# Kernel optimization log

Measured on AMD Instinct MI355X. Metric: run time of the kernel, lower is better.

The kernel has to match this reference:

```python
import jax, jax.numpy as jnp
import numpy as np

N = 100000      # number of entities
E = 400000      # number of edges (before self-loops)
D = 200         # feature_dim
D0 = 100        # init_fea_dim
NREL = 475      # 2*num_rels + 1 (self-loop relation = NREL-1)
NBR = 100       # num_base_r
B = 1024        # query batch
L = 2           # number of cells / layers
EPS = 1e-5


def _bn(x, g, b):
    # BatchNorm1d, training-mode batch statistics (biased var), per-feature affine
    m = jnp.mean(x, axis=0)
    v = jnp.var(x, axis=0)
    return (x - m) * jax.lax.rsqrt(v + EPS) * g + b


def setup_inputs() -> dict:
    key = jax.random.key(0)
    ks = jax.random.split(key, 12)
    return {
        # graph (edge list form of the DGL graph g)
        "src_id": jax.random.randint(ks[0], (E,), 0, N),
        "dst_id": jax.random.randint(ks[1], (E,), 0, N),
        "e_type": jax.random.randint(ks[2], (E,), 0, NREL - 1),  # NREL-1 reserved for self-loop
        # link-prediction queries
        "subj": jax.random.randint(ks[3], (B,), 0, N),
        "rel": jax.random.randint(ks[4], (B,), 0, NREL),
        # learned parameters
        "emb_h": jax.random.normal(ks[5], (N, D0), dtype=jnp.float32) * 0.02,
        "emb_e": jax.random.normal(ks[6], (NBR, D), dtype=jnp.float32) * 0.1,
        "lin_w": jax.random.normal(ks[7], (D0, D), dtype=jnp.float32) * (1.0 / np.sqrt(D0)),
        "lin_b": jnp.zeros((D,), dtype=jnp.float32),
        "rel_wt": jax.random.normal(ks[8], (NREL, NBR), dtype=jnp.float32) * 0.1,
        "w_rel": jax.random.normal(ks[9], (D, D), dtype=jnp.float32) * (1.0 / np.sqrt(D)),
        # per-cell params, stacked over L layers
        "agg_bn_g": jnp.ones((L, D), dtype=jnp.float32),
        "agg_bn_b": jnp.zeros((L, D), dtype=jnp.float32),
        "cell_bn_g": jnp.ones((L, D), dtype=jnp.float32),
        "cell_bn_b": jnp.zeros((L, D), dtype=jnp.float32),
        "concat_w": jax.random.normal(ks[10], (L, D, D), dtype=jnp.float32) * (1.0 / np.sqrt(D)),
        "concat_b": jnp.zeros((L, D), dtype=jnp.float32),
    }


def reference(src_id, dst_id, e_type, subj, rel,
              emb_h, emb_e, lin_w, lin_b, rel_wt, w_rel,
              agg_bn_g, agg_bn_b, cell_bn_g, cell_bn_b, concat_w, concat_b):
    nodes = jnp.arange(N, dtype=src_id.dtype)
    # append self-loops for every node, with the dedicated self-loop relation id
    src_f = jnp.concatenate([src_id, nodes])                      # [E+N]
    dst_f = jnp.concatenate([dst_id, nodes])                      # [E+N]
    et_f = jnp.concatenate([e_type, jnp.full((N,), NREL - 1, dtype=e_type.dtype)])

    all_ent = emb_h @ lin_w + lin_b                               # [N, D]
    rel_embed = rel_wt @ emb_e                                    # [NREL, D]

    for i in range(L):
        src_emb = all_ent[src_f]                                  # [E+N, D] per-edge gather
        hr = rel_embed[et_f]                                      # [E+N, D] per-edge gather
        zero_out = src_emb * hr                                   # pre_mult op (no BN/ReLU)
        agg = jax.ops.segment_sum(zero_out, dst_f, num_segments=N)  # edge -> node aggregation
        agg = jax.nn.relu(_bn(agg, agg_bn_g[i], agg_bn_b[i]))     # OpModule BN + ReLU
        h = agg @ concat_w[i] + concat_b[i]                       # Cell concat Linear (1 concat node)
        all_ent = jax.nn.relu(_bn(h, cell_bn_g[i], cell_bn_b[i]))  # Cell BN + ReLU
        rel_embed = rel_embed @ w_rel                             # per-layer relation transform

    # DistMult score function: [B, N]
    score = (all_ent[subj] * rel_embed[rel]) @ all_ent.T
    return score
```

## Files before the change

kernel.cpp:

```cpp
#include <hip/hip_runtime.h>


#define N_ENT  100000
#define N_EDGE 400000
#define D_     200
#define D0_    100
#define NREL_  475
#define B_     1024
#define GSTAT2 2048
#define KP_D   224
#define KP_D0  128

typedef unsigned short ushort_t;
typedef __attribute__((ext_vector_type(8))) short bf16x8;
typedef __attribute__((ext_vector_type(4))) float f32x4;

__device__ __forceinline__ ushort_t f2bf(float x) {
  unsigned u = __float_as_uint(x);
  return (ushort_t)((u + 0x7FFFu + ((u >> 16) & 1u)) >> 16);
}
__device__ __forceinline__ float bf2f(ushort_t h) {
  return __uint_as_float(((unsigned)h) << 16);
}

__device__ __forceinline__ void gld16(const void* g, void* l) {
  __builtin_amdgcn_global_load_lds(
      (const __attribute__((address_space(1))) unsigned*)g,
      (__attribute__((address_space(3))) unsigned*)l, 16, 0, 0);
}


__global__ void k_hist(const int* __restrict__ dst_id, int* __restrict__ cnt) {
  int e = blockIdx.x * 256 + threadIdx.x;
  if (e < N_EDGE) atomicAdd(&cnt[dst_id[e]], 1);
}

__global__ __launch_bounds__(256) void k_scan_block(const int* __restrict__ cnt,
                                                    int* __restrict__ rp,
                                                    int* __restrict__ bsum) {
  __shared__ int sm[256];
  int tid = threadIdx.x;
  int base = blockIdx.x * 1024 + tid * 4;
  int v0 = (base + 0 < N_ENT) ? cnt[base + 0] : 0;
  int v1 = (base + 1 < N_ENT) ? cnt[base + 1] : 0;
  int v2 = (base + 2 < N_ENT) ? cnt[base + 2] : 0;
  int v3 = (base + 3 < N_ENT) ? cnt[base + 3] : 0;
  int tsum = v0 + v1 + v2 + v3;
  sm[tid] = tsum;
  __syncthreads();
  for (int off = 1; off < 256; off <<= 1) {
    int t = (tid >= off) ? sm[tid - off] : 0;
    __syncthreads();
    sm[tid] += t;
    __syncthreads();
  }
  int run = sm[tid] - tsum;
  if (base + 0 < N_ENT) { rp[base + 0] = run; } run += v0;
  if (base + 1 < N_ENT) { rp[base + 1] = run; } run += v1;
  if (base + 2 < N_ENT) { rp[base + 2] = run; } run += v2;
  if (base + 3 < N_ENT) { rp[base + 3] = run; }
  if (tid == 255) bsum[blockIdx.x] = sm[255];
}

__global__ void k_scan_tops(int* __restrict__ bsum, int nb) {
  __shared__ int sm[256];
  int tid = threadIdx.x;
  int v = (tid < nb) ? bsum[tid] : 0;
  sm[tid] = v;
  __syncthreads();
  for (int off = 1; off < 256; off <<= 1) {
    int t = (tid >= off) ? sm[tid - off] : 0;
    __syncthreads();
    sm[tid] += t;
    __syncthreads();
  }
  if (tid < nb) bsum[tid] = sm[tid] - v;
}

__global__ void k_scan_add(int* __restrict__ rp, const int* __restrict__ bsum,
                           int* __restrict__ cursor) {
  int i = blockIdx.x * 256 + threadIdx.x;
  if (i < N_ENT) {
    int r = rp[i] + bsum[i >> 10];
    rp[i] = r;
    cursor[i] = r;
  }
}

__global__ void k_fill(const int* __restrict__ src_id, const int* __restrict__ dst_id,
                       const int* __restrict__ e_type, int* __restrict__ cursor,
                       int* __restrict__ cs, int* __restrict__ ct) {
  int e = blockIdx.x * 256 + threadIdx.x;
  if (e < N_EDGE) {
    int pos = atomicAdd(&cursor[dst_id[e]], 1);
    cs[pos] = src_id[e];
    ct[pos] = e_type[e];
  }
}


template <bool BN>
__global__ __launch_bounds__(256) void k_aggregate(const float* __restrict__ ent,
                                                   const float* __restrict__ relE,
                                                   const int* __restrict__ rp,
                                                   const int* __restrict__ cnt,
                                                   const int* __restrict__ cs,
                                                   const int* __restrict__ ct,
                                                   float* __restrict__ out,
                                                   const float* __restrict__ scale,
                                                   const float* __restrict__ shift) {
  const int wv = threadIdx.x >> 6;
  const int lane = threadIdx.x & 63;
  const int n = blockIdx.x * 4 + wv;
  if (n >= N_ENT || lane >= 50) return;
  const int f4 = lane * 4;

  float sc[4] = {0, 0, 0, 0}, sh[4] = {0, 0, 0, 0};
  if (BN) {
    float4 s4 = *(const float4*)(scale + f4);
    float4 h4 = *(const float4*)(shift + f4);
    sc[0] = s4.x; sc[1] = s4.y; sc[2] = s4.z; sc[3] = s4.w;
    sh[0] = h4.x; sh[1] = h4.y; sh[2] = h4.z; sh[3] = h4.w;
  }

  float ax[4], ay[4] = {0, 0, 0, 0};
  {
    float4 e = *(const float4*)(ent + (long)n * D_ + f4);
    float4 r = *(const float4*)(relE + (long)(NREL_ - 1) * D_ + f4);
    float ee[4] = {e.x, e.y, e.z, e.w};
    float rr[4] = {r.x, r.y, r.z, r.w};
#pragma unroll
    for (int u = 0; u < 4; ++u) {
      if (BN) ee[u] = fmaxf(fmaf(ee[u], sc[u], sh[u]), 0.f);
      ax[u] = ee[u] * rr[u];
    }
  }

  int s0 = rp[n], e0 = s0 + cnt[n];
  int idx = s0;
  for (; idx + 2 <= e0; idx += 2) {
    int sA = cs[idx], tA = ct[idx];
    int sB = cs[idx + 1], tB = ct[idx + 1];
    float4 eA = *(const float4*)(ent + (long)sA * D_ + f4);
    float4 rA = *(const float4*)(relE + (long)tA * D_ + f4);
    float4 eB = *(const float4*)(ent + (long)sB * D_ + f4);
    float4 rB = *(const float4*)(relE + (long)tB * D_ + f4);
    float ea[4] = {eA.x, eA.y, eA.z, eA.w}, ra[4] = {rA.x, rA.y, rA.z, rA.w};
    float eb[4] = {eB.x, eB.y, eB.z, eB.w}, rb[4] = {rB.x, rB.y, rB.z, rB.w};
#pragma unroll
    for (int u = 0; u < 4; ++u) {
      if (BN) {
        ea[u] = fmaxf(fmaf(ea[u], sc[u], sh[u]), 0.f);
        eb[u] = fmaxf(fmaf(eb[u], sc[u], sh[u]), 0.f);
      }
      ax[u] = fmaf(ea[u], ra[u], ax[u]);
      ay[u] = fmaf(eb[u], rb[u], ay[u]);
    }
  }
  if (idx < e0) {
    int sA = cs[idx], tA = ct[idx];
    float4 eA = *(const float4*)(ent + (long)sA * D_ + f4);
    float4 rA = *(const float4*)(relE + (long)tA * D_ + f4);
    float ea[4] = {eA.x, eA.y, eA.z, eA.w}, ra[4] = {rA.x, rA.y, rA.z, rA.w};
#pragma unroll
    for (int u = 0; u < 4; ++u) {
      if (BN) ea[u] = fmaxf(fmaf(ea[u], sc[u], sh[u]), 0.f);
      ax[u] = fmaf(ea[u], ra[u], ax[u]);
    }
  }
  float4 o = make_float4(ax[0] + ay[0], ax[1] + ay[1], ax[2] + ay[2], ax[3] + ay[3]);
  *(float4*)(out + (long)n * D_ + f4) = o;
}

__global__ __launch_bounds__(64) void k_colstats(const float* __restrict__ X,
                                                 double* __restrict__ part) {
  int t = threadIdx.x;
  if (t >= 50) return;
  double s0 = 0, s1 = 0, s2 = 0, s3 = 0, q0 = 0, q1 = 0, q2 = 0, q3 = 0;
  for (int r = blockIdx.x; r < N_ENT; r += GSTAT2) {
    float4 v = *(const float4*)(X + (long)r * D_ + t * 4);
    s0 += v.x; q0 += (double)v.x * v.x;
    s1 += v.y; q1 += (double)v.y * v.y;
    s2 += v.z; q2 += (double)v.z * v.z;
    s3 += v.w; q3 += (double)v.w * v.w;
  }
  long o = (long)blockIdx.x * 400 + t * 4;
  part[o + 0] = s0; part[o + 1] = s1; part[o + 2] = s2; part[o + 3] = s3;
  part[o + 200] = q0; part[o + 201] = q1; part[o + 202] = q2; part[o + 203] = q3;
}

__global__ __launch_bounds__(256) void k_bn_fin(const double* __restrict__ part,
                                                const float* __restrict__ g,
                                                const float* __restrict__ b,
                                                float* __restrict__ scale,
                                                float* __restrict__ shift) {
  int f = blockIdx.x;
  int tid = threadIdx.x;
  double S = 0.0, S2 = 0.0;
  for (int i = tid; i < GSTAT2; i += 256) {
    S += part[(long)i * 400 + f];
    S2 += part[(long)i * 400 + 200 + f];
  }
  __shared__ double smS[256], smS2[256];
  smS[tid] = S; smS2[tid] = S2;
  __syncthreads();
  for (int off = 128; off > 0; off >>= 1) {
    if (tid < off) { smS[tid] += smS[tid + off]; smS2[tid] += smS2[tid + off]; }
    __syncthreads();
  }
  if (tid == 0) {
    double mean = smS[0] / N_ENT;
    double var = smS2[0] / N_ENT - mean * mean;
    double inv = 1.0 / sqrt(var + 1e-5);
    float sc = g[f] * (float)inv;
    scale[f] = sc;
    shift[f] = b[f] - (float)mean * sc;
  }
}

__global__ void k_norm_split(float* __restrict__ X, const float* __restrict__ scale,
                             const float* __restrict__ shift,
                             ushort_t* __restrict__ H, ushort_t* __restrict__ L) {
  const long total = (long)N_ENT * (KP_D / 4);
  for (long i4 = (long)blockIdx.x * 256 + threadIdx.x; i4 < total;
       i4 += (long)gridDim.x * 256) {
    int r = (int)(i4 / (KP_D / 4));
    int c4 = (int)(i4 % (KP_D / 4)) * 4;
    float vv[4] = {0.f, 0.f, 0.f, 0.f};
    if (c4 < D_) {
      float4 v = *(float4*)(X + (long)r * D_ + c4);
      vv[0] = fmaxf(fmaf(v.x, scale[c4 + 0], shift[c4 + 0]), 0.f);
      vv[1] = fmaxf(fmaf(v.y, scale[c4 + 1], shift[c4 + 1]), 0.f);
      vv[2] = fmaxf(fmaf(v.z, scale[c4 + 2], shift[c4 + 2]), 0.f);
      vv[3] = fmaxf(fmaf(v.w, scale[c4 + 3], shift[c4 + 3]), 0.f);
      *(float4*)(X + (long)r * D_ + c4) = make_float4(vv[0], vv[1], vv[2], vv[3]);
    }
    ushort_t h[4], l[4];
#pragma unroll
    for (int t = 0; t < 4; t++) {
      h[t] = f2bf(vv[t]);
      l[t] = f2bf(vv[t] - bf2f(h[t]));
    }
    long o = (long)r * KP_D + c4;
    *(uint2*)(H + o) = make_uint2((unsigned)h[0] | ((unsigned)h[1] << 16),
                                  (unsigned)h[2] | ((unsigned)h[3] << 16));
    *(uint2*)(L + o) = make_uint2((unsigned)l[0] | ((unsigned)l[1] << 16),
                                  (unsigned)l[2] | ((unsigned)l[3] << 16));
  }
}

__global__ void k_tsplit(const float* __restrict__ W, int K, int Nc, int Kp,
                         ushort_t* __restrict__ H, ushort_t* __restrict__ L) {
  int i = blockIdx.x * 256 + threadIdx.x;
  if (i >= Nc * Kp) return;
  int n = i / Kp, kp = i - n * Kp;
  float v = (kp < K) ? W[(long)kp * Nc + n] : 0.f;
  ushort_t h = f2bf(v);
  H[i] = h;
  L[i] = f2bf(v - bf2f(h));
}

__global__ void k_qsplit(const float* __restrict__ ent, const float* __restrict__ relE,
                         const int* __restrict__ subj, const int* __restrict__ rel,
                         ushort_t* __restrict__ H, ushort_t* __restrict__ L) {
  int i = blockIdx.x * 256 + threadIdx.x;
  if (i >= B_ * KP_D) return;
  int b = i / KP_D, kp = i - b * KP_D;
  float v = 0.f;
  if (kp < D_)
    v = ent[(long)subj[b] * D_ + kp] * relE[(long)rel[b] * D_ + kp];
  ushort_t h = f2bf(v);
  H[i] = h;
  L[i] = f2bf(v - bf2f(h));
}

__global__ __launch_bounds__(256, 2) void k_score4(
    const ushort_t* __restrict__ Ah, const ushort_t* __restrict__ Al,
    const ushort_t* __restrict__ Bh, const ushort_t* __restrict__ Bl,
    float* __restrict__ C) {
  constexpr int KP = KP_D;
  __shared__ __align__(16) ushort_t lds[2 * 14336];
  const int tid = threadIdx.x;
  const int wave = tid >> 6, lane = tid & 63;
  const int l15 = lane & 15, l4 = lane >> 4;

  int g = (blockIdx.x & 7) * 1563 + (blockIdx.x >> 3);
  const int bm = (g & 7) * 128;
  const int bn = (g >> 3) * 64;

  bf16x8 qh[2][7], ql[2][7];
#pragma unroll
  for (int i = 0; i < 2; ++i) {
    long rowa = (long)(bm + wave * 32 + i * 16 + l15) * KP + l4 * 8;
#pragma unroll
    for (int k = 0; k < 7; ++k) {
      qh[i][k] = *(const bf16x8*)(Ah + rowa + k * 32);
      ql[i][k] = *(const bf16x8*)(Al + rowa + k * 32);
    }
  }

#pragma unroll
  for (int jj = 0; jj < 14; ++jj) {
    int c = wave * 14 + jj;
    int u = c * 64 + lane;
    int isl = (u >= 1792) ? 1 : 0;
    int u2 = u - isl * 1792;
    int kst = u2 >> 8;
    int rem = u2 & 255;
    int r = rem >> 2;
    int slot = rem & 3;
    int srcslot = slot ^ ((r >> 1) & 3);
    int rowg = bn + r; if (rowg > N_ENT - 1) rowg = N_ENT - 1;
    const ushort_t* src = (isl ? Bl : Bh) + (long)rowg * KP + kst * 32 + srcslot * 8;
    gld16(src, lds + c * 512);
  }
  __syncthreads();

  f32x4 acc[2][4] = {};
#pragma unroll
  for (int k = 0; k < 7; ++k) {
    bf16x8 eh[4], el[4];
#pragma unroll
    for (int j = 0; j < 4; ++j) {
      int rB = j * 16 + l15;
      int slot = l4 ^ ((rB >> 1) & 3);
      int ad = k * 2048 + rB * 32 + slot * 8;
      eh[j] = *(const bf16x8*)(lds + ad);
      el[j] = *(const bf16x8*)(lds + 14336 + ad);
    }
#pragma unroll
    for (int i = 0; i < 2; ++i)
#pragma unroll
      for (int j = 0; j < 4; ++j) {
        acc[i][j] = __builtin_amdgcn_mfma_f32_16x16x32_bf16(eh[j], qh[i][k], acc[i][j], 0, 0, 0);
        acc[i][j] = __builtin_amdgcn_mfma_f32_16x16x32_bf16(eh[j], ql[i][k], acc[i][j], 0, 0, 0);
        acc[i][j] = __builtin_amdgcn_mfma_f32_16x16x32_bf16(el[j], qh[i][k], acc[i][j], 0, 0, 0);
      }
  }

#pragma unroll
  for (int i = 0; i < 2; ++i) {
    int m = bm + wave * 32 + i * 16 + l15;
#pragma unroll
    for (int j = 0; j < 4; ++j) {
      int nb = bn + j * 16 + l4 * 4;
      if (nb < N_ENT) {
        float4 o = make_float4(acc[i][j][0], acc[i][j][1], acc[i][j][2], acc[i][j][3]);
        *(float4*)(C + (long)m * N_ENT + nb) = o;
      }
    }
  }
}

template <bool BN_A, bool HAS_BIAS>
__global__ __launch_bounds__(256, 2) void k_mfma_af32(
    const float* __restrict__ A, int lda, int K,
    const ushort_t* __restrict__ Bh, const ushort_t* __restrict__ Bl,
    float* __restrict__ C, int M, int Nc, int Kp, long ldc,
    const float* __restrict__ scale, const float* __restrict__ shift,
    const float* __restrict__ bias) {
  __shared__ __align__(16) ushort_t lds[2 * 16384];
  __shared__ float sc_lds[KP_D], sh_lds[KP_D];
  const int tid = threadIdx.x;
  const int wave = tid >> 6, lane = tid & 63;
  const int bm = blockIdx.x * 128, bn = blockIdx.y * 128;
  const int wr = (wave >> 1) * 64, wc = (wave & 1) * 64;
  const int l15 = lane & 15, l4 = lane >> 4;
  const int NT = Kp >> 5;

  if (BN_A) {
    for (int i = tid; i < Kp; i += 256) {
      sc_lds[i] = (i < K) ? scale[i] : 0.f;
      sh_lds[i] = (i < K) ? shift[i] : 0.f;
    }
    __syncthreads();
  }

  const int ar = tid >> 1;
  const int acb = (tid & 1) * 16;
  int arow = bm + ar; if (arow > M - 1) arow = M - 1;
  const int aswz = (ar >> 1) & 3;
  const int s0 = (((acb >> 3) + 0) ^ aswz) * 8;
  const int s1 = (((acb >> 3) + 1) ^ aswz) * 8;

  auto loadA = [&](int kt, float4* va) {
    int kc = kt * 32 + acb;
    const float* ap = A + (long)arow * lda + kc;
    if (kc + 16 <= K) {
#pragma unroll
      for (int q = 0; q < 4; q++) va[q] = *(const float4*)(ap + q * 4);
    } else {
#pragma unroll
      for (int q = 0; q < 4; q++) {
        float t0 = (kc + q * 4 + 0 < K) ? ap[q * 4 + 0] : 0.f;
        float t1 = (kc + q * 4 + 1 < K) ? ap[q * 4 + 1] : 0.f;
        float t2 = (kc + q * 4 + 2 < K) ? ap[q * 4 + 2] : 0.f;
        float t3 = (kc + q * 4 + 3 < K) ? ap[q * 4 + 3] : 0.f;
        va[q] = make_float4(t0, t1, t2, t3);
      }
    }
  };

  auto writeA = [&](int kt, int ph, float4* va) {
    float v[16];
#pragma unroll
    for (int q = 0; q < 4; q++) {
      v[q * 4 + 0] = va[q].x; v[q * 4 + 1] = va[q].y;
      v[q * 4 + 2] = va[q].z; v[q * 4 + 3] = va[q].w;
    }
    if (BN_A) {
      int kc = kt * 32 + acb;
#pragma unroll
      for (int e = 0; e < 16; e++) {
        int col = kc + e;
        if (col < K) v[e] = fmaxf(fmaf(v[e], sc_lds[col], sh_lds[col]), 0.f);
      }
    }
    unsigned hh[8], ll[8];
#pragma unroll
    for (int e = 0; e < 8; e++) {
      ushort_t h0 = f2bf(v[2 * e]), h1 = f2bf(v[2 * e + 1]);
      ushort_t l0 = f2bf(v[2 * e] - bf2f(h0)), l1 = f2bf(v[2 * e + 1] - bf2f(h1));
      hh[e] = (unsigned)h0 | ((unsigned)h1 << 16);
      ll[e] = (unsigned)l0 | ((unsigned)l1 << 16);
    }
    ushort_t* baseA = lds + ph * 16384 + ar * 32;
    *(uint4*)(baseA + s0) = make_uint4(hh[0], hh[1], hh[2], hh[3]);
    *(uint4*)(baseA + s1) = make_uint4(hh[4], hh[5], hh[6], hh[7]);
    ushort_t* baseL = baseA + 4096;
    *(uint4*)(baseL + s0) = make_uint4(ll[0], ll[1], ll[2], ll[3]);
    *(uint4*)(baseL + s1) = make_uint4(ll[4], ll[5], ll[6], ll[7]);
  };

  auto stageB = [&](int kt, int ph) {
#pragma unroll
    for (int j = 0; j < 4; ++j) {
      int c = 16 + wave * 4 + j;
      int buf = c >> 3;
      int r = (c & 7) * 16 + (lane >> 2);
      int sg = (lane & 3) ^ ((r >> 1) & 3);
      const ushort_t* bp = (buf == 2) ? Bh : Bl;
      int rowg = bn + r; if (rowg > Nc - 1) rowg = Nc - 1;
      gld16(bp + (long)rowg * Kp + kt * 32 + sg * 8, lds + ph * 16384 + c * 512);
    }
  };

  f32x4 acc[4][4] = {};
  {
    float4 va[4];
    loadA(0, va);
    writeA(0, 0, va);
    stageB(0, 0);
  }
  __syncthreads();
  int p = 0;
  for (int t = 0; t < NT; ++t) {
    float4 va[4];
    const bool pre = (t + 1 < NT);
    if (pre) {
      loadA(t + 1, va);
      stageB(t + 1, p ^ 1);
    }
    const ushort_t* base = lds + p * 16384;
    bf16x8 a_h[4], a_l[4], b_h[4], b_l[4];
#pragma unroll
    for (int i = 0; i < 4; i++) {
      int rA = wr + i * 16 + l15;
      int sA = (l4 ^ ((rA >> 1) & 3)) * 8;
      a_h[i] = *(const bf16x8*)(base + rA * 32 + sA);
      a_l[i] = *(const bf16x8*)(base + 4096 + rA * 32 + sA);
      int rB = wc + i * 16 + l15;
      int sB = (l4 ^ ((rB >> 1) & 3)) * 8;
      b_h[i] = *(const bf16x8*)(base + 8192 + rB * 32 + sB);
      b_l[i] = *(const bf16x8*)(base + 12288 + rB * 32 + sB);
    }
#pragma unroll
    for (int i = 0; i < 4; i++)
#pragma unroll
      for (int j = 0; j < 4; j++) {
        acc[i][j] = __builtin_amdgcn_mfma_f32_16x16x32_bf16(a_h[i], b_h[j], acc[i][j], 0, 0, 0);
        acc[i][j] = __builtin_amdgcn_mfma_f32_16x16x32_bf16(a_l[i], b_h[j], acc[i][j], 0, 0, 0);
        acc[i][j] = __builtin_amdgcn_mfma_f32_16x16x32_bf16(a_h[i], b_l[j], acc[i][j], 0, 0, 0);
      }
    if (pre) writeA(t + 1, p ^ 1, va);
    __syncthreads();
    p ^= 1;
  }

#pragma unroll
  for (int i = 0; i < 4; i++) {
    int mrow = bm + wr + i * 16 + l4 * 4;
#pragma unroll
    for (int j = 0; j < 4; j++) {
      int n = bn + wc + j * 16 + l15;
      if (n >= Nc) continue;
      float bb = HAS_BIAS ? bias[n] : 0.f;
#pragma unroll
      for (int v = 0; v < 4; v++) {
        int m = mrow + v;
        if (m < M) C[(long)m * ldc + n] = acc[i][j][v] + bb;
      }
    }
  }
}

template <int TM, int TN>
__global__ __launch_bounds__(256) void k_gemm_abt(
    const float* __restrict__ A, const float* __restrict__ Bm, float* __restrict__ C,
    int M, int Nc, int K, long ldc) {
  constexpr int BM = TM * 16, BN = TN * 16, KC = 20;
  __shared__ float As[BM * KC];
  __shared__ float Bs[BN * KC];
  const int tid = threadIdx.x;
  const int tx = tid & 15, ty = tid >> 4;
  const int bm = blockIdx.x * BM, bn = blockIdx.y * BN;
  float acc[TM][TN];
#pragma unroll
  for (int i = 0; i < TM; i++)
#pragma unroll
    for (int j = 0; j < TN; j++) acc[i][j] = 0.f;
  for (int kc = 0; kc < K; kc += KC) {
    for (int i4 = tid; i4 < BM * 5; i4 += 256) {
      int r = i4 / 5, kq = (i4 - r * 5) * 4;
      int row = bm + r; if (row > M - 1) row = M - 1;
      *(float4*)(As + r * KC + kq) = *(const float4*)(A + (long)row * K + kc + kq);
    }
    for (int i4 = tid; i4 < BN * 5; i4 += 256) {
      int r = i4 / 5, kq = (i4 - r * 5) * 4;
      int row = bn + r; if (row > Nc - 1) row = Nc - 1;
      *(float4*)(Bs + r * KC + kq) = *(const float4*)(Bm + (long)row * K + kc + kq);
    }
    __syncthreads();
#pragma unroll
    for (int k4 = 0; k4 < KC; k4 += 4) {
      float4 af[TM], bf[TN];
#pragma unroll
      for (int i = 0; i < TM; i++) af[i] = *(const float4*)(As + (i * 16 + ty) * KC + k4);
#pragma unroll
      for (int j = 0; j < TN; j++) bf[j] = *(const float4*)(Bs + (j * 16 + tx) * KC + k4);
#pragma unroll
      for (int i = 0; i < TM; i++)
#pragma unroll
        for (int j = 0; j < TN; j++) {
          acc[i][j] = fmaf(af[i].x, bf[j].x, acc[i][j]);
          acc[i][j] = fmaf(af[i].y, bf[j].y, acc[i][j]);
          acc[i][j] = fmaf(af[i].z, bf[j].z, acc[i][j]);
          acc[i][j] = fmaf(af[i].w, bf[j].w, acc[i][j]);
        }
    }
    __syncthreads();
  }
#pragma unroll
  for (int i = 0; i < TM; i++) {
    int m = bm + i * 16 + ty;
    if (m >= M) continue;
#pragma unroll
    for (int j = 0; j < TN; j++) {
      int n = bn + j * 16 + tx;
      if (n < Nc) C[(long)m * ldc + n] = acc[i][j];
    }
  }
}

__global__ void k_transpose(const float* __restrict__ s, float* __restrict__ d, int R, int C) {
  int i = blockIdx.x * 256 + threadIdx.x;
  if (i < R * C) { int r = i / C, c = i - r * C; d[c * R + r] = s[i]; }
}


extern "C" void kernel_launch(void* const* d_in, const int* in_sizes, int n_in,
                              void* d_out, int out_size, void* d_ws, size_t ws_size,
                              hipStream_t stream) {
  const int* src_id = (const int*)d_in[0];
  const int* dst_id = (const int*)d_in[1];
  const int* e_type = (const int*)d_in[2];
  const int* subj = (const int*)d_in[3];
  const int* rel = (const int*)d_in[4];
  const float* emb_h = (const float*)d_in[5];
  const float* emb_e = (const float*)d_in[6];
  const float* lin_w = (const float*)d_in[7];
  const float* lin_b = (const float*)d_in[8];
  const float* rel_wt = (const float*)d_in[9];
  const float* w_rel = (const float*)d_in[10];
  const float* agg_bn_g = (const float*)d_in[11];
  const float* agg_bn_b = (const float*)d_in[12];
  const float* cell_bn_g = (const float*)d_in[13];
  const float* cell_bn_b = (const float*)d_in[14];
  const float* concat_w = (const float*)d_in[15];
  const float* concat_b = (const float*)d_in[16];
  float* out = (float*)d_out;

  char* w = (char*)d_ws;
  ushort_t* ent_h = (ushort_t*)(w + 0);
  ushort_t* ent_l = (ushort_t*)(w + 44800000);
  ushort_t* q_h   = (ushort_t*)(w + 89600000);
  ushort_t* q_l   = (ushort_t*)(w + 90112000);

  char* ob = (char*)d_out;
  float* ent    = (float*)(ob + 0);
  float* tmp    = (float*)(ob + 80000000);
  double* part  = (double*)(ob + 160000000);
  int* counts   = (int*)(ob + 166600000);
  int* row_ptr  = (int*)(ob + 167000000);
  int* cursor   = (int*)(ob + 167400000);
  int* csr_src  = (int*)(ob + 167800000);
  int* csr_et   = (int*)(ob + 169400000);
  float* relA   = (float*)(ob + 171800000);
  float* relB   = (float*)(ob + 172180000);
  float* embeT  = (float*)(ob + 172560000);
  float* wrT    = (float*)(ob + 172640000);
  ushort_t* linw_h = (ushort_t*)(ob + 172800000);
  ushort_t* linw_l = (ushort_t*)(ob + 172851200);
  ushort_t* cw0_h  = (ushort_t*)(ob + 172902400);
  ushort_t* cw0_l  = (ushort_t*)(ob + 172992000);
  ushort_t* cw1_h  = (ushort_t*)(ob + 173081600);
  ushort_t* cw1_l  = (ushort_t*)(ob + 173171200);
  float* scaleb = (float*)(ob + 173260800);
  float* shiftb = (float*)(ob + 173261824);
  int* bsum     = (int*)(ob + 173262848);

  (void)hipMemsetAsync(counts, 0, N_ENT * sizeof(int), stream);
  k_hist<<<(N_EDGE + 255) / 256, 256, 0, stream>>>(dst_id, counts);
  const int NB = (N_ENT + 1023) / 1024;
  k_scan_block<<<NB, 256, 0, stream>>>(counts, row_ptr, bsum);
  k_scan_tops<<<1, 256, 0, stream>>>(bsum, NB);
  k_scan_add<<<(N_ENT + 255) / 256, 256, 0, stream>>>(row_ptr, bsum, cursor);
  k_fill<<<(N_EDGE + 255) / 256, 256, 0, stream>>>(src_id, dst_id, e_type, cursor,
                                                   csr_src, csr_et);

  k_tsplit<<<(D_ * KP_D0 + 255) / 256, 256, 0, stream>>>(lin_w, D0_, D_, KP_D0,
                                                         linw_h, linw_l);
  k_tsplit<<<(D_ * KP_D + 255) / 256, 256, 0, stream>>>(concat_w, D_, D_, KP_D,
                                                        cw0_h, cw0_l);
  k_tsplit<<<(D_ * KP_D + 255) / 256, 256, 0, stream>>>(concat_w + D_ * D_, D_, D_,
                                                        KP_D, cw1_h, cw1_l);
  k_transpose<<<(D0_ * D_ + 255) / 256, 256, 0, stream>>>(emb_e, embeT, D0_, D_);
  k_transpose<<<(D_ * D_ + 255) / 256, 256, 0, stream>>>(w_rel, wrT, D_, D_);

  const int GM = (N_ENT + 127) / 128;
  const int GA = (N_ENT + 3) / 4;

  k_mfma_af32<false, true><<<dim3(GM, 2), 256, 0, stream>>>(
      emb_h, D0_, D0_, linw_h, linw_l, ent, N_ENT, D_, KP_D0, (long)D_,
      nullptr, nullptr, lin_b);
  k_gemm_abt<8, 4><<<dim3(4, 4), 256, 0, stream>>>(rel_wt, embeT, relA, NREL_, D_,
                                                   D0_, (long)D_);

  k_aggregate<false><<<GA, 256, 0, stream>>>(ent, relA, row_ptr, counts,
                                             csr_src, csr_et, tmp, nullptr, nullptr);
  k_colstats<<<GSTAT2, 64, 0, stream>>>(tmp, part);
  k_bn_fin<<<D_, 256, 0, stream>>>(part, agg_bn_g, agg_bn_b, scaleb, shiftb);
  k_mfma_af32<true, true><<<dim3(GM, 2), 256, 0, stream>>>(
      tmp, D_, D_, cw0_h, cw0_l, ent, N_ENT, D_, KP_D, (long)D_,
      scaleb, shiftb, concat_b);
  k_colstats<<<GSTAT2, 64, 0, stream>>>(ent, part);
  k_bn_fin<<<D_, 256, 0, stream>>>(part, cell_bn_g, cell_bn_b, scaleb, shiftb);
  k_gemm_abt<8, 4><<<dim3(4, 4), 256, 0, stream>>>(relA, wrT, relB, NREL_, D_, D_,
                                                   (long)D_);

  k_aggregate<true><<<GA, 256, 0, stream>>>(ent, relB, row_ptr, counts,
                                            csr_src, csr_et, tmp, scaleb, shiftb);
  k_colstats<<<GSTAT2, 64, 0, stream>>>(tmp, part);
  k_bn_fin<<<D_, 256, 0, stream>>>(part, agg_bn_g + D_, agg_bn_b + D_, scaleb, shiftb);
  k_mfma_af32<true, true><<<dim3(GM, 2), 256, 0, stream>>>(
      tmp, D_, D_, cw1_h, cw1_l, ent, N_ENT, D_, KP_D, (long)D_,
      scaleb, shiftb, concat_b + D_);
  k_colstats<<<GSTAT2, 64, 0, stream>>>(ent, part);
  k_bn_fin<<<D_, 256, 0, stream>>>(part, cell_bn_g + D_, cell_bn_b + D_, scaleb, shiftb);
  k_norm_split<<<2048, 256, 0, stream>>>(ent, scaleb, shiftb, ent_h, ent_l);
  k_gemm_abt<8, 4><<<dim3(4, 4), 256, 0, stream>>>(relB, wrT, relA, NREL_, D_, D_,
                                                   (long)D_);

  k_qsplit<<<(B_ * KP_D + 255) / 256, 256, 0, stream>>>(ent, relA, subj, rel,
                                                        q_h, q_l);

  k_score4<<<dim3(8 * 1563), 256, 0, stream>>>(q_h, q_l, ent_h, ent_l, out);
}
```

Baseline: 1.027 ms.

## Drop fp32 writeback in norm_split and software-pipeline score kernel query loads

The final-layer BN+ReLU no longer writes the normalized fp32 entity matrix back to memory. k_qsplit instead applies scale/shift/ReLU itself to the few gathered subject rows. The score kernel stops preloading all 14 query fragments per row group into registers. It double-buffers them per k-step and adds sched_group_barrier hints to interleave global loads, LDS reads and MFMAs, which cuts register pressure and a large fp32 store.

```diff
diff --git a/kernel.cpp b/kernel.cpp
--- a/kernel.cpp
+++ b/kernel.cpp
@@ -218,7 +218,8 @@
   }
 }
 
-__global__ void k_norm_split(float* __restrict__ X, const float* __restrict__ scale,
+__global__ void k_norm_split(const float* __restrict__ X,
+                             const float* __restrict__ scale,
                              const float* __restrict__ shift,
                              ushort_t* __restrict__ H, ushort_t* __restrict__ L) {
   const long total = (long)N_ENT * (KP_D / 4);
@@ -228,12 +229,11 @@
     int c4 = (int)(i4 % (KP_D / 4)) * 4;
     float vv[4] = {0.f, 0.f, 0.f, 0.f};
     if (c4 < D_) {
-      float4 v = *(float4*)(X + (long)r * D_ + c4);
+      float4 v = *(const float4*)(X + (long)r * D_ + c4);
       vv[0] = fmaxf(fmaf(v.x, scale[c4 + 0], shift[c4 + 0]), 0.f);
       vv[1] = fmaxf(fmaf(v.y, scale[c4 + 1], shift[c4 + 1]), 0.f);
       vv[2] = fmaxf(fmaf(v.z, scale[c4 + 2], shift[c4 + 2]), 0.f);
       vv[3] = fmaxf(fmaf(v.w, scale[c4 + 3], shift[c4 + 3]), 0.f);
-      *(float4*)(X + (long)r * D_ + c4) = make_float4(vv[0], vv[1], vv[2], vv[3]);
     }
     ushort_t h[4], l[4];
 #pragma unroll
@@ -262,19 +262,23 @@
 
 __global__ void k_qsplit(const float* __restrict__ ent, const float* __restrict__ relE,
                          const int* __restrict__ subj, const int* __restrict__ rel,
+                         const float* __restrict__ scale, const float* __restrict__ shift,
                          ushort_t* __restrict__ H, ushort_t* __restrict__ L) {
   int i = blockIdx.x * 256 + threadIdx.x;
   if (i >= B_ * KP_D) return;
   int b = i / KP_D, kp = i - b * KP_D;
   float v = 0.f;
-  if (kp < D_)
-    v = ent[(long)subj[b] * D_ + kp] * relE[(long)rel[b] * D_ + kp];
+  if (kp < D_) {
+    float e = ent[(long)subj[b] * D_ + kp];
+    e = fmaxf(fmaf(e, scale[kp], shift[kp]), 0.f);
+    v = e * relE[(long)rel[b] * D_ + kp];
+  }
   ushort_t h = f2bf(v);
   H[i] = h;
   L[i] = f2bf(v - bf2f(h));
 }
 
-__global__ __launch_bounds__(256, 2) void k_score4(
+__global__ __launch_bounds__(256, 2) void k_score6(
     const ushort_t* __restrict__ Ah, const ushort_t* __restrict__ Al,
     const ushort_t* __restrict__ Bh, const ushort_t* __restrict__ Bl,
     float* __restrict__ C) {
@@ -288,16 +292,12 @@
   const int bm = (g & 7) * 128;
   const int bn = (g >> 3) * 64;
 
-  bf16x8 qh[2][7], ql[2][7];
-#pragma unroll
-  for (int i = 0; i < 2; ++i) {
-    long rowa = (long)(bm + wave * 32 + i * 16 + l15) * KP + l4 * 8;
-#pragma unroll
-    for (int k = 0; k < 7; ++k) {
-      qh[i][k] = *(const bf16x8*)(Ah + rowa + k * 32);
-      ql[i][k] = *(const bf16x8*)(Al + rowa + k * 32);
-    }
-  }
+  const long rowa0 = (long)(bm + wave * 32 + 0 * 16 + l15) * KP + l4 * 8;
+  const long rowa1 = (long)(bm + wave * 32 + 1 * 16 + l15) * KP + l4 * 8;
+  const ushort_t* pa0 = Ah + rowa0;
+  const ushort_t* pa1 = Ah + rowa1;
+  const ushort_t* pl0 = Al + rowa0;
+  const ushort_t* pl1 = Al + rowa1;
 
 #pragma unroll
   for (int jj = 0; jj < 14; ++jj) {
@@ -314,29 +314,57 @@
     const ushort_t* src = (isl ? Bl : Bh) + (long)rowg * KP + kst * 32 + srcslot * 8;
     gld16(src, lds + c * 512);
   }
+
+  bf16x8 Aqh0, Aqh1, Aql0, Aql1, Bqh0, Bqh1, Bql0, Bql1;
+#define QLOAD(P, k)                                  \
+  P##qh0 = *(const bf16x8*)(pa0 + (k) * 32);         \
+  P##qh1 = *(const bf16x8*)(pa1 + (k) * 32);         \
+  P##ql0 = *(const bf16x8*)(pl0 + (k) * 32);         \
+  P##ql1 = *(const bf16x8*)(pl1 + (k) * 32);
+
+  QLOAD(A, 0)
   __syncthreads();
 
   f32x4 acc[2][4] = {};
-#pragma unroll
-  for (int k = 0; k < 7; ++k) {
-    bf16x8 eh[4], el[4];
-#pragma unroll
-    for (int j = 0; j < 4; ++j) {
-      int rB = j * 16 + l15;
-      int slot = l4 ^ ((rB >> 1) & 3);
-      int ad = k * 2048 + rB * 32 + slot * 8;
-      eh[j] = *(const bf16x8*)(lds + ad);
-      el[j] = *(const bf16x8*)(lds + 14336 + ad);
-    }
-#pragma unroll
-    for (int i = 0; i < 2; ++i)
-#pragma unroll
-      for (int j = 0; j < 4; ++j) {
-        acc[i][j] = __builtin_amdgcn_mfma_f32_16x16x32_bf16(eh[j], qh[i][k], acc[i][j], 0, 0, 0);
-        acc[i][j] = __builtin_amdgcn_mfma_f32_16x16x32_bf16(eh[j], ql[i][k], acc[i][j], 0, 0, 0);
-        acc[i][j] = __builtin_amdgcn_mfma_f32_16x16x32_bf16(el[j], qh[i][k], acc[i][j], 0, 0, 0);
-      }
-  }
+#define KSTEP(k, P)                                                            \
+  {                                                                            \
+    bf16x8 eh[4], el[4];                                                       \
+    _Pragma("unroll") for (int j = 0; j < 4; ++j) {                            \
+      int rB = j * 16 + l15;                                                   \
+      int slot = l4 ^ ((rB >> 1) & 3);                                         \
+      int ad = (k) * 2048 + rB * 32 + slot * 8;                                \
+      eh[j] = *(const bf16x8*)(lds + ad);                                      \
+      el[j] = *(const bf16x8*)(lds + 14336 + ad);                              \
+    }                                                                          \
+    _Pragma("unroll") for (int j = 0; j < 4; ++j) {                            \
+      acc[0][j] = __builtin_amdgcn_mfma_f32_16x16x32_bf16(eh[j], P##qh0, acc[0][j], 0, 0, 0); \
+      acc[0][j] = __builtin_amdgcn_mfma_f32_16x16x32_bf16(eh[j], P##ql0, acc[0][j], 0, 0, 0); \
+      acc[0][j] = __builtin_amdgcn_mfma_f32_16x16x32_bf16(el[j], P##qh0, acc[0][j], 0, 0, 0); \
+      acc[1][j] = __builtin_amdgcn_mfma_f32_16x16x32_bf16(eh[j], P##qh1, acc[1][j], 0, 0, 0); \
+      acc[1][j] = __builtin_amdgcn_mfma_f32_16x16x32_bf16(eh[j], P##ql1, acc[1][j], 0, 0, 0); \
+      acc[1][j] = __builtin_amdgcn_mfma_f32_16x16x32_bf16(el[j], P##qh1, acc[1][j], 0, 0, 0); \
+    }                                                                          \
+  }
+#define SGB_FULL                                          \
+  __builtin_amdgcn_sched_group_barrier(0x20, 4, 0);       \
+  __builtin_amdgcn_sched_group_barrier(0x100, 8, 0);      \
+  __builtin_amdgcn_sched_group_barrier(0x8, 24, 0);
+#define SGB_TAIL                                          \
+  __builtin_amdgcn_sched_group_barrier(0x100, 8, 0);      \
+  __builtin_amdgcn_sched_group_barrier(0x8, 24, 0);
+
+  QLOAD(B, 1) KSTEP(0, A) SGB_FULL
+  QLOAD(A, 2) KSTEP(1, B) SGB_FULL
+  QLOAD(B, 3) KSTEP(2, A) SGB_FULL
+  QLOAD(A, 4) KSTEP(3, B) SGB_FULL
+  QLOAD(B, 5) KSTEP(4, A) SGB_FULL
+  QLOAD(A, 6) KSTEP(5, B) SGB_FULL
+  KSTEP(6, A) SGB_TAIL
+
+#undef QLOAD
+#undef KSTEP
+#undef SGB_FULL
+#undef SGB_TAIL
 
 #pragma unroll
   for (int i = 0; i < 2; ++i) {
@@ -672,7 +700,7 @@
                                                    (long)D_);
 
   k_qsplit<<<(B_ * KP_D + 255) / 256, 256, 0, stream>>>(ent, relA, subj, rel,
-                                                        q_h, q_l);
-
-  k_score4<<<dim3(8 * 1563), 256, 0, stream>>>(q_h, q_l, ent_h, ent_l, out);
-}
+                                                        scaleb, shiftb, q_h, q_l);
+
+  k_score6<<<dim3(8 * 1563), 256, 0, stream>>>(q_h, q_l, ent_h, ent_l, out);
+}
```

Result: no change. 1.030 ms (+0.3%).
